# Optimization experiments

Measured on AMD Instinct MI355X. Metric: run time of the kernel, lower is better.

Reference implementation:

```python
import jax, jax.numpy as jnp
import numpy as np

NUM_BINS = 15
N = 33_554_432  # number of samples


def setup_inputs() -> dict:
    key = jax.random.key(0)
    k1, k2 = jax.random.split(key)
    probs = jax.random.uniform(k1, (N,), dtype=jnp.float32)
    labels = jax.random.randint(k2, (N,), 0, 2, dtype=jnp.int32)
    return {"probs": probs, "labels": labels}


def reference(probs, labels):
    # bins = linspace(0,1,NUM_BINS+1); element falls in bin b iff
    # probs > b/NUM_BINS and probs <= (b+1)/NUM_BINS  =>  b = ceil(p*NUM_BINS)-1.
    n = probs.shape[0]
    idx = jnp.clip(jnp.ceil(probs * NUM_BINS).astype(jnp.int32) - 1, 0, NUM_BINS - 1)
    # elements with probs <= 0 or > 1 fall in no bin (strict lower on bin 0)
    valid = (probs > 0.0) & (probs <= 1.0)
    w = valid.astype(probs.dtype)
    counts = jax.ops.segment_sum(w, idx, num_segments=NUM_BINS)
    sum_conf = jax.ops.segment_sum(probs * w, idx, num_segments=NUM_BINS)
    sum_acc = jax.ops.segment_sum(labels.astype(probs.dtype) * w, idx, num_segments=NUM_BINS)
    denom = jnp.maximum(counts, 1.0)  # safe divide; empty bins contribute 0
    avg_conf = sum_conf / denom
    avg_acc = sum_acc / denom
    ece = jnp.sum((counts / n) * jnp.abs(avg_acc - avg_conf))
    return ece
```

## Files before the change

kernel.cpp:

```cpp
#include <hip/hip_runtime.h>

#define NUM_BINS 15
#define NBLOCKS 1024
#define NTHREADS 256
#define NCOMP (3 * NUM_BINS)

__global__ __launch_bounds__(NTHREADS) void ece_partial(
    const float* __restrict__ probs, const int* __restrict__ labels,
    float* __restrict__ ws, int n4)
{
    float cnt[NUM_BINS], conf[NUM_BINS], acc[NUM_BINS];
#pragma unroll
    for (int b = 0; b < NUM_BINS; ++b) { cnt[b] = 0.f; conf[b] = 0.f; acc[b] = 0.f; }

    const float4* __restrict__ p4 = (const float4*)probs;
    const int4*   __restrict__ l4 = (const int4*)labels;

    const int stride = gridDim.x * blockDim.x;
    for (int i = blockIdx.x * blockDim.x + threadIdx.x; i < n4; i += stride) {
        float4 p = p4[i];
        int4   l = l4[i];
        float ps[4] = {p.x, p.y, p.z, p.w};
        int   ls[4] = {l.x, l.y, l.z, l.w};
#pragma unroll
        for (int e = 0; e < 4; ++e) {
            float pv = ps[e];
            float lf = (float)ls[e];
            int bin = (int)ceilf(pv * 15.0f) - 1;
            bin = min(max(bin, 0), NUM_BINS - 1);
            if (!((pv > 0.0f) && (pv <= 1.0f))) bin = -1;
#pragma unroll
            for (int b = 0; b < NUM_BINS; ++b) {
                float w = (bin == b) ? 1.0f : 0.0f;
                cnt[b]  += w;
                conf[b]  = fmaf(w, pv, conf[b]);
                acc[b]   = fmaf(w, lf, acc[b]);
            }
        }
    }

#pragma unroll
    for (int b = 0; b < NUM_BINS; ++b) {
#pragma unroll
        for (int off = 32; off; off >>= 1) {
            cnt[b]  += __shfl_down(cnt[b],  off);
            conf[b] += __shfl_down(conf[b], off);
            acc[b]  += __shfl_down(acc[b],  off);
        }
    }

    __shared__ float red[NTHREADS / 64][NCOMP];
    const int wave = threadIdx.x >> 6;
    const int lane = threadIdx.x & 63;
    if (lane == 0) {
#pragma unroll
        for (int b = 0; b < NUM_BINS; ++b) {
            red[wave][b]                = cnt[b];
            red[wave][NUM_BINS + b]     = conf[b];
            red[wave][2 * NUM_BINS + b] = acc[b];
        }
    }
    __syncthreads();
    if (threadIdx.x < NCOMP) {
        float s = 0.f;
#pragma unroll
        for (int w = 0; w < NTHREADS / 64; ++w) s += red[w][threadIdx.x];
        ws[threadIdx.x * gridDim.x + blockIdx.x] = s;
    }
}

__global__ __launch_bounds__(1024) void ece_final(
    const float* __restrict__ ws, float* __restrict__ out, int nblocks, float n)
{
    __shared__ float sums[NCOMP];
    const int wave   = threadIdx.x >> 6;
    const int lane   = threadIdx.x & 63;
    const int nwaves = blockDim.x >> 6;

    for (int c = wave; c < NCOMP; c += nwaves) {
        float s = 0.f;
        for (int i = lane; i < nblocks; i += 64) s += ws[c * nblocks + i];
#pragma unroll
        for (int off = 32; off; off >>= 1) s += __shfl_down(s, off);
        if (lane == 0) sums[c] = s;
    }
    __syncthreads();

    if (threadIdx.x == 0) {
        float ece = 0.f;
#pragma unroll
        for (int b = 0; b < NUM_BINS; ++b) {
            float c  = sums[b];
            float cf = sums[NUM_BINS + b];
            float ac = sums[2 * NUM_BINS + b];
            float denom = fmaxf(c, 1.0f);
            ece += (c / n) * fabsf(ac / denom - cf / denom);
        }
        out[0] = ece;
    }
}

extern "C" void kernel_launch(void* const* d_in, const int* in_sizes, int n_in,
                              void* d_out, int out_size, void* d_ws, size_t ws_size,
                              hipStream_t stream)
{
    const float* probs  = (const float*)d_in[0];
    const int*   labels = (const int*)d_in[1];
    float*       out    = (float*)d_out;
    float*       ws     = (float*)d_ws;

    const int n  = in_sizes[0];
    const int n4 = n / 4;

    ece_partial<<<NBLOCKS, NTHREADS, 0, stream>>>(probs, labels, ws, n4);
    ece_final<<<1, 1024, 0, stream>>>(ws, out, NBLOCKS, (float)n);
}
```

Baseline: 296.4 us.

## Replace one-hot register accumulation with per-thread LDS histograms and packed count/label

Each element previously ran a 15-bin one-hot loop of three FMAs per bin. Now each thread does two LDS atomic adds into its own private shared-memory column. The count and the label sum share one float (1 + label/1024) and are split later with floor, and out-of-range elements go to a discarded 16th bin. This cuts per-element ALU work so the kernel can get closer to memory bandwidth, at the cost of LDS traffic. It depends on per-thread counts staying small enough that the packed fraction stays exact, and the final kernel now hardcodes the block count.

```diff
diff --git a/kernel.cpp b/kernel.cpp
--- a/kernel.cpp
+++ b/kernel.cpp
@@ -1,87 +1,115 @@
 #include <hip/hip_runtime.h>
 
 #define NUM_BINS 15
-#define NBLOCKS 1024
-#define NTHREADS 256
-#define NCOMP (3 * NUM_BINS)
+#define NB 1024
+#define NT 256
+#define NROWS 32
+#define NCOMP 45
 
-__global__ __launch_bounds__(NTHREADS) void ece_partial(
+__device__ __forceinline__ void accum(float* hist, int t, float pv, int lv) {
+    int bin = (int)ceilf(pv * 15.0f) - 1;
+    bin = min(max(bin, -1), 15);
+    bin &= 15;
+    float v0 = fmaf((float)lv, 0.0009765625f, 1.0f);
+    atomicAdd(&hist[(bin << 8) + t], v0);
+    atomicAdd(&hist[((bin + 16) << 8) + t], pv);
+}
+
+__global__ __launch_bounds__(NT) void ece_partial(
     const float* __restrict__ probs, const int* __restrict__ labels,
     float* __restrict__ ws, int n4)
 {
-    float cnt[NUM_BINS], conf[NUM_BINS], acc[NUM_BINS];
+    __shared__ float hist[NROWS * NT];
+    const int t = threadIdx.x;
+
+    float4* h4 = (float4*)hist;
 #pragma unroll
-    for (int b = 0; b < NUM_BINS; ++b) { cnt[b] = 0.f; conf[b] = 0.f; acc[b] = 0.f; }
+    for (int i = 0; i < (NROWS * NT / 4) / NT; ++i)
+        h4[i * NT + t] = float4{0.f, 0.f, 0.f, 0.f};
+    __syncthreads();
 
     const float4* __restrict__ p4 = (const float4*)probs;
     const int4*   __restrict__ l4 = (const int4*)labels;
+    const int tid    = blockIdx.x * NT + t;
+    const int stride = gridDim.x * NT;
 
-    const int stride = gridDim.x * blockDim.x;
-    for (int i = blockIdx.x * blockDim.x + threadIdx.x; i < n4; i += stride) {
+    const int iters = n4 / stride;
+#pragma unroll 4
+    for (int k = 0; k < iters; ++k) {
+        const int i = tid + k * stride;
         float4 p = p4[i];
         int4   l = l4[i];
-        float ps[4] = {p.x, p.y, p.z, p.w};
-        int   ls[4] = {l.x, l.y, l.z, l.w};
-#pragma unroll
-        for (int e = 0; e < 4; ++e) {
-            float pv = ps[e];
-            float lf = (float)ls[e];
-            int bin = (int)ceilf(pv * 15.0f) - 1;
-            bin = min(max(bin, 0), NUM_BINS - 1);
-            if (!((pv > 0.0f) && (pv <= 1.0f))) bin = -1;
-#pragma unroll
-            for (int b = 0; b < NUM_BINS; ++b) {
-                float w = (bin == b) ? 1.0f : 0.0f;
-                cnt[b]  += w;
-                conf[b]  = fmaf(w, pv, conf[b]);
-                acc[b]   = fmaf(w, lf, acc[b]);
-            }
-        }
+        accum(hist, t, p.x, l.x);
+        accum(hist, t, p.y, l.y);
+        accum(hist, t, p.z, l.z);
+        accum(hist, t, p.w, l.w);
     }
-
-#pragma unroll
-    for (int b = 0; b < NUM_BINS; ++b) {
-#pragma unroll
-        for (int off = 32; off; off >>= 1) {
-            cnt[b]  += __shfl_down(cnt[b],  off);
-            conf[b] += __shfl_down(conf[b], off);
-            acc[b]  += __shfl_down(acc[b],  off);
-        }
-    }
-
-    __shared__ float red[NTHREADS / 64][NCOMP];
-    const int wave = threadIdx.x >> 6;
-    const int lane = threadIdx.x & 63;
-    if (lane == 0) {
-#pragma unroll
-        for (int b = 0; b < NUM_BINS; ++b) {
-            red[wave][b]                = cnt[b];
-            red[wave][NUM_BINS + b]     = conf[b];
-            red[wave][2 * NUM_BINS + b] = acc[b];
+    {
+        const int i = tid + iters * stride;
+        if (i < n4) {
+            float4 p = p4[i];
+            int4   l = l4[i];
+            accum(hist, t, p.x, l.x);
+            accum(hist, t, p.y, l.y);
+            accum(hist, t, p.z, l.z);
+            accum(hist, t, p.w, l.w);
         }
     }
     __syncthreads();
-    if (threadIdx.x < NCOMP) {
-        float s = 0.f;
+
+    const int r = t >> 3, s = t & 7;
+    const float4* rp4 = (const float4*)(hist + (r << 8) + (s << 5));
+    if (r < 16) {
+        float csum = 0.f, asum = 0.f;
 #pragma unroll
-        for (int w = 0; w < NTHREADS / 64; ++w) s += red[w][threadIdx.x];
-        ws[threadIdx.x * gridDim.x + blockIdx.x] = s;
+        for (int k = 0; k < 8; ++k) {
+            float4 v = rp4[k];
+            float c0 = floorf(v.x), c1 = floorf(v.y), c2 = floorf(v.z), c3 = floorf(v.w);
+            csum += (c0 + c1) + (c2 + c3);
+            asum += ((v.x - c0) + (v.y - c1)) + ((v.z - c2) + (v.w - c3));
+        }
+        asum *= 1024.f;
+#pragma unroll
+        for (int o = 4; o; o >>= 1) {
+            csum += __shfl_down(csum, o);
+            asum += __shfl_down(asum, o);
+        }
+        if (s == 0 && r < NUM_BINS) {
+            ws[r * NB + blockIdx.x]              = csum;
+            ws[(NUM_BINS + r) * NB + blockIdx.x] = asum;
+        }
+    } else {
+        float fsum = 0.f;
+#pragma unroll
+        for (int k = 0; k < 8; ++k) {
+            float4 v = rp4[k];
+            fsum += (v.x + v.y) + (v.z + v.w);
+        }
+#pragma unroll
+        for (int o = 4; o; o >>= 1) fsum += __shfl_down(fsum, o);
+        const int b = r - 16;
+        if (s == 0 && b < NUM_BINS)
+            ws[(2 * NUM_BINS + b) * NB + blockIdx.x] = fsum;
     }
 }
 
 __global__ __launch_bounds__(1024) void ece_final(
-    const float* __restrict__ ws, float* __restrict__ out, int nblocks, float n)
+    const float* __restrict__ ws, float* __restrict__ out, float n)
 {
     __shared__ float sums[NCOMP];
-    const int wave   = threadIdx.x >> 6;
-    const int lane   = threadIdx.x & 63;
-    const int nwaves = blockDim.x >> 6;
+    const int wave = threadIdx.x >> 6;
+    const int lane = threadIdx.x & 63;
 
-    for (int c = wave; c < NCOMP; c += nwaves) {
+    for (int c = wave; c < NCOMP; c += 16) {
+        const float4* row4 = (const float4*)(ws + c * NB);
         float s = 0.f;
-        for (int i = lane; i < nblocks; i += 64) s += ws[c * nblocks + i];
 #pragma unroll
-        for (int off = 32; off; off >>= 1) s += __shfl_down(s, off);
+        for (int k = 0; k < NB / 256; ++k) {
+            float4 v = row4[lane + (k << 6)];
+            s += (v.x + v.y) + (v.z + v.w);
+        }
+#pragma unroll
+        for (int o = 32; o; o >>= 1) s += __shfl_down(s, o);
         if (lane == 0) sums[c] = s;
     }
     __syncthreads();
@@ -90,11 +118,11 @@
         float ece = 0.f;
 #pragma unroll
         for (int b = 0; b < NUM_BINS; ++b) {
-            float c  = sums[b];
-            float cf = sums[NUM_BINS + b];
-            float ac = sums[2 * NUM_BINS + b];
-            float denom = fmaxf(c, 1.0f);
-            ece += (c / n) * fabsf(ac / denom - cf / denom);
+            float cnt = sums[b];
+            float acc = sums[NUM_BINS + b];
+            float cf  = sums[2 * NUM_BINS + b];
+            float denom = fmaxf(cnt, 1.f);
+            ece += (cnt / n) * fabsf(acc / denom - cf / denom);
         }
         out[0] = ece;
     }
@@ -106,12 +134,8 @@
 {
     const float* probs  = (const float*)d_in[0];
     const int*   labels = (const int*)d_in[1];
-    float*       out    = (float*)d_out;
-    float*       ws     = (float*)d_ws;
+    const int n = in_sizes[0];
 
-    const int n  = in_sizes[0];
-    const int n4 = n / 4;
-
-    ece_partial<<<NBLOCKS, NTHREADS, 0, stream>>>(probs, labels, ws, n4);
-    ece_final<<<1, 1024, 0, stream>>>(ws, out, NBLOCKS, (float)n);
+    ece_partial<<<NB, NT, 0, stream>>>(probs, labels, (float*)d_ws, n / 4);
+    ece_final<<<1, 1024, 0, stream>>>((const float*)d_ws, (float*)d_out, (float)n);
 }
```

Measured after the change: 522.7 us. 76.3% more time.
